# Kernel optimization log

Measured on AMD Instinct MI355X. Metric: run time of the kernel, lower is better.

## Reference

```python
import jax, jax.numpy as jnp
import numpy as np
from jax import lax

B, S, T = 32, 128, 128
V_SRC, V_TGT, E, U = 32000, 32000, 128, 256


def _lstm(xs, h0, c0, Wx, Wh, b):
    # xs: [T, B, F]; Keras gate order i, f, g(candidate), o
    def step(carry, x):
        h, c = carry
        z = x @ Wx + h @ Wh + b
        i, f, g, o = jnp.split(z, 4, axis=-1)
        c = jax.nn.sigmoid(f) * c + jax.nn.sigmoid(i) * jnp.tanh(g)
        h = jax.nn.sigmoid(o) * jnp.tanh(c)
        return (h, c), h
    (h, c), hs = lax.scan(step, (h0, c0), xs)
    return hs, h, c


def setup_inputs() -> dict:
    key = jax.random.key(0)
    ks = jax.random.split(key, 20)
    p = lambda k, shp: (jax.random.normal(k, shp, dtype=jnp.float32) * 0.02)
    return {
        "src": jax.random.randint(ks[0], (B, S), 0, V_SRC),
        "tgt": jax.random.randint(ks[1], (B, T), 0, V_TGT),
        "enc_emb": p(ks[2], (V_SRC, E)),
        "enc_Wx": p(ks[3], (E, 4 * U)),
        "enc_Wh": p(ks[4], (U, 4 * U)),
        "enc_b": jnp.zeros((4 * U,), jnp.float32),
        "dec_emb": p(ks[5], (V_TGT, E)),
        "dec_Wx": p(ks[6], (U + E, 4 * U)),
        "dec_Wh": p(ks[7], (U, 4 * U)),
        "dec_b": jnp.zeros((4 * U,), jnp.float32),
        "att_W1": p(ks[8], (U, U)),
        "att_b1": jnp.zeros((U,), jnp.float32),
        "att_W2": p(ks[9], (U, U)),
        "att_b2": jnp.zeros((U,), jnp.float32),
        "att_V": p(ks[10], (U, 1)),
        "att_bV": jnp.zeros((1,), jnp.float32),
        "fc_W": p(ks[11], (U, V_TGT)),
        "fc_b": jnp.zeros((V_TGT,), jnp.float32),
    }


def reference(src, tgt, enc_emb, enc_Wx, enc_Wh, enc_b, dec_emb, dec_Wx, dec_Wh,
              dec_b, att_W1, att_b1, att_W2, att_b2, att_V, att_bV, fc_W, fc_b):
    # ---- encoder ----
    enc_x = enc_emb[src]                                  # [B,S,E]
    enc_hs, h, c = _lstm(enc_x.transpose(1, 0, 2),
                         jnp.zeros((B, U), enc_Wx.dtype),
                         jnp.zeros((B, U), enc_Wx.dtype),
                         enc_Wx, enc_Wh, enc_b)
    enc_out = enc_hs.transpose(1, 0, 2)                   # [B,S,U]
    keys = enc_out @ att_W2 + att_b2                      # [B,S,U] (hoisted, same math)

    # ---- decoder (faithful: step 0 uses tgt[:,0]; step t>=1 uses tgt[:,t-1]) ----
    dec_tokens = jnp.concatenate([tgt[:, :1], tgt[:, :-1]], axis=1)  # [B,T]
    dec_x = dec_emb[dec_tokens].transpose(1, 0, 2)        # [T,B,E]

    def step(carry, x_emb):
        h, c = carry
        q = (h @ att_W1 + att_b1)[:, None, :]             # [B,1,U]
        score = jnp.tanh(q + keys) @ att_V + att_bV       # [B,S,1]
        attn = jax.nn.softmax(score, axis=1)
        ctx = jnp.sum(attn * enc_out, axis=1)             # [B,U]
        xin = jnp.concatenate([ctx, x_emb], axis=-1)      # [B,U+E]
        z = xin @ dec_Wx + h @ dec_Wh + dec_b
        i, f, g, o = jnp.split(z, 4, axis=-1)
        c = jax.nn.sigmoid(f) * c + jax.nn.sigmoid(i) * jnp.tanh(g)
        h = jax.nn.sigmoid(o) * jnp.tanh(c)
        probs = jax.nn.softmax(h @ fc_W + fc_b, axis=-1)  # [B,V]
        return (h, c), probs

    _, out = lax.scan(step, (h, c), dec_x)                # [T,B,V]
    return out.transpose(1, 0, 2)                         # [B,T,V]
```

## Files before the change

kernel.cpp:

```cpp
#include <hip/hip_runtime.h>
#include <hip/hip_bf16.h>
#include <hip/hip_fp16.h>
#include <cstdint>
#include <cstddef>

#define B_ 32
#define S_ 128
#define T_ 128
#define E_ 128
#define U_ 256
#define V_ 32000
#define G4 1024
#define TV 4096000

typedef __attribute__((ext_vector_type(8))) short short8_t;
typedef __attribute__((ext_vector_type(4))) float f32x4;
typedef unsigned long long u64;

static __device__ __forceinline__ unsigned short f2bf(float x) {
  union { float f; unsigned int u; } v; v.f = x;
  unsigned int r = (v.u + 0x7fffu + ((v.u >> 16) & 1u)) >> 16;
  return (unsigned short)r;
}
static __device__ __forceinline__ float sigmoidf_(float x) {
  return 1.0f / (1.0f + __expf(-x));
}
static __device__ __forceinline__ float tanhf_(float x) {
  float e = __expf(2.0f * x);
  return 1.0f - 2.0f / (e + 1.0f);
}

static __device__ __forceinline__ unsigned int f2e5(float x) {
  __half h = __float2half(x);
  __half_raw hr = *(__half_raw*)&h;
  unsigned int u = hr.x;
  unsigned int r = (u + 0x7Fu + ((u >> 8) & 1u)) >> 8;
  return r & 0xFFu;
}

static __device__ __forceinline__ unsigned pk2(float a, float b) {
  auto h = __builtin_amdgcn_cvt_pkrtz(a, b);
  return __builtin_bit_cast(unsigned, h);
}
#define SEL01 0x05000400u
#define SEL23 0x07000600u
static __device__ __forceinline__ unsigned e5pair(unsigned w, unsigned sel) {
  return __builtin_amdgcn_perm(w, 0u, sel);
}
static __device__ __forceinline__ float dot2(unsigned a, unsigned b, float c) {
  float d;
  asm("v_dot2_f32_f16 %0, %1, %2, %3" : "=v"(d) : "v"(a), "v"(b), "v"(c));
  return d;
}
static __device__ __forceinline__ unsigned pkadd(unsigned a, unsigned b) {
  unsigned d; asm("v_pk_add_f16 %0, %1, %2" : "=v"(d) : "v"(a), "v"(b)); return d;
}
static __device__ __forceinline__ unsigned pkmul(unsigned a, unsigned b) {
  unsigned d; asm("v_pk_mul_f16 %0, %1, %2" : "=v"(d) : "v"(a), "v"(b)); return d;
}
static __device__ __forceinline__ unsigned pkfma(unsigned a, unsigned b, unsigned c) {
  unsigned d; asm("v_pk_fma_f16 %0, %1, %2, %3" : "=v"(d) : "v"(a), "v"(b), "v"(c)); return d;
}
static __device__ __forceinline__ unsigned pkmax(unsigned a, unsigned b) {
  unsigned d; asm("v_pk_max_f16 %0, %1, %2" : "=v"(d) : "v"(a), "v"(b)); return d;
}
static __device__ __forceinline__ unsigned pkmin(unsigned a, unsigned b) {
  unsigned d; asm("v_pk_min_f16 %0, %1, %2" : "=v"(d) : "v"(a), "v"(b)); return d;
}

static __device__ __forceinline__ void pub64u(u64* p, unsigned val, unsigned tag) {
  u64 v = ((u64)tag << 32) | (u64)val;
  __hip_atomic_store(p, v, __ATOMIC_RELAXED, __HIP_MEMORY_SCOPE_AGENT);
}
static __device__ __forceinline__ u64 ld64(const u64* p) {
  return __hip_atomic_load(p, __ATOMIC_RELAXED, __HIP_MEMORY_SCOPE_AGENT);
}

__global__ __launch_bounds__(256) void k_prep_x(
    const int* __restrict__ src, const int* __restrict__ tgt,
    const float* __restrict__ enc_emb, const float* __restrict__ enc_Wx,
    const float* __restrict__ enc_b,
    const float* __restrict__ dec_emb, const float* __restrict__ dec_Wx,
    const float* __restrict__ dec_b,
    float* __restrict__ Xe, float* __restrict__ Xd)
{
  __shared__ float emb_l[8][E_];
  int wg = blockIdx.x;
  int tid = threadIdx.x;
  bool is_dec = (wg >= 512);
  int r0 = (is_dec ? (wg - 512) : wg) * 8;
  const float* emb  = is_dec ? dec_emb : enc_emb;
  const float* W    = is_dec ? (dec_Wx + (size_t)U_ * G4) : enc_Wx;
  const float* bias = is_dec ? dec_b : enc_b;
  float* Xout = is_dec ? Xd : Xe;

  for (int i = 0; i < 4; ++i) {
    int lin = i * 256 + tid;
    int rr = lin >> 7, k = lin & 127;
    int r = r0 + rr;
    int b = r & 31, st = r >> 5;
    int tok;
    if (is_dec) tok = tgt[b * T_ + (st > 0 ? st - 1 : 0)];
    else        tok = src[b * S_ + st];
    emb_l[rr][k] = emb[(size_t)tok * E_ + k];
  }
  __syncthreads();

  float acc[8][4];
  #pragma unroll
  for (int rr = 0; rr < 8; ++rr)
    #pragma unroll
    for (int cc = 0; cc < 4; ++cc) acc[rr][cc] = 0.f;

  for (int k = 0; k < E_; ++k) {
    float w0 = W[(size_t)k * G4 + tid];
    float w1 = W[(size_t)k * G4 + tid + 256];
    float w2 = W[(size_t)k * G4 + tid + 512];
    float w3 = W[(size_t)k * G4 + tid + 768];
    #pragma unroll
    for (int rr = 0; rr < 8; ++rr) {
      float e = emb_l[rr][k];
      acc[rr][0] += e * w0; acc[rr][1] += e * w1;
      acc[rr][2] += e * w2; acc[rr][3] += e * w3;
    }
  }
  #pragma unroll
  for (int rr = 0; rr < 8; ++rr) {
    int r = r0 + rr;
    #pragma unroll
    for (int cc = 0; cc < 4; ++cc) {
      int col = tid + cc * 256;
      Xout[(size_t)r * G4 + col] = acc[rr][cc] + bias[col];
    }
  }
}

__global__ __launch_bounds__(256) void k_prep_fcw(
    const float* __restrict__ fcW, unsigned short* __restrict__ fcWt)
{
  __shared__ float tile[64][65];
  int bid = blockIdx.x, tid = threadIdx.x;
  int n0 = (bid % 500) * 64, k0 = (bid / 500) * 64;
  for (int i = 0; i < 16; ++i) {
    int lin = i * 256 + tid;
    int k = lin >> 6, n = lin & 63;
    tile[k][n] = fcW[(size_t)(k0 + k) * V_ + n0 + n];
  }
  __syncthreads();
  for (int i = 0; i < 16; ++i) {
    int lin = i * 256 + tid;
    int n = lin >> 6, k = lin & 63;
    fcWt[(size_t)(n0 + n) * 256 + k0 + k] = f2bf(tile[k][n]);
  }
}

__global__ __launch_bounds__(1024) void k_encoder8(
    const float* __restrict__ Xe, const float* __restrict__ Wh,
    float* __restrict__ enc_out, float* __restrict__ h_state,
    float* __restrict__ c_state, u64* __restrict__ hpubE )
{
  __shared__ unsigned int WhU[64 * 128];
  __shared__ unsigned int h2[128];
  __shared__ float scr_z[8 * 128];

  int bid = blockIdx.x, tid = threadIdx.x;
  int b = bid & 31, g = bid >> 5;

  for (int idx = tid; idx < 64 * 128; idx += 1024) {
    int k4 = idx >> 7, c = idx & 127;
    int gc = (c >> 5) * 256 + g * 32 + (c & 31);
    unsigned w = 0;
    #pragma unroll
    for (int i = 0; i < 4; ++i)
      w |= f2e5(Wh[(size_t)(4 * k4 + i) * G4 + gc]) << (8 * i);
    WhU[k4 * 128 + c] = w;
  }
  float c_reg = 0.f, h_reg = 0.f;
  __syncthreads();

  for (int s = 0; s < S_; ++s) {
    float xe0 = 0.f, xe1 = 0.f, xe2 = 0.f, xe3 = 0.f;
    if (tid < 32) {
      const float* xe = Xe + (size_t)(s * B_ + b) * G4 + g * 32 + tid;
      xe0 = xe[0]; xe1 = xe[256]; xe2 = xe[512]; xe3 = xe[768];
    }
    if (tid < 128) {
      if (s == 0) h2[tid] = 0u;
      else {
        const u64* p = &hpubE[((size_t)(s & 1) * 32 + b) * 128 + tid];
        u64 v = ld64(p);
        while ((unsigned)(v >> 32) < (unsigned)s) { __builtin_amdgcn_s_sleep(1); v = ld64(p); }
        h2[tid] = (unsigned)v;
      }
    }
    __syncthreads();
    {
      int c = tid & 127, k8 = tid >> 7;
      const unsigned* wp = &WhU[(k8 * 8) * 128 + c];
      const unsigned* hh = &h2[k8 * 16];
      float z0 = 0.f, z1 = 0.f;
      #pragma unroll
      for (int j = 0; j < 8; ++j) {
        unsigned w = wp[j * 128];
        z0 = dot2(e5pair(w, SEL01), hh[2 * j], z0);
        z1 = dot2(e5pair(w, SEL23), hh[2 * j + 1], z1);
      }
      scr_z[k8 * 128 + c] = z0 + z1;
    }
    __syncthreads();
    if (tid < 32) {
      int r = tid, gc = g * 32 + r;
      float z[4] = {xe0, xe1, xe2, xe3};
      #pragma unroll
      for (int q = 0; q < 4; ++q) {
        int c = q * 32 + r;
        #pragma unroll
        for (int k8 = 0; k8 < 8; ++k8) z[q] += scr_z[k8 * 128 + c];
      }
      float c = sigmoidf_(z[1]) * c_reg + sigmoidf_(z[0]) * tanhf_(z[2]);
      c_reg = c;
      float h = sigmoidf_(z[3]) * tanhf_(c);
      h_reg = h;
      enc_out[((size_t)(b * S_ + s)) * U_ + gc] = h;
      if (s < S_ - 1) {
        float hx = __shfl_xor(h, 1);
        if (!(r & 1))
          pub64u(&hpubE[((size_t)((s + 1) & 1) * 32 + b) * 128 + g * 16 + (r >> 1)],
                 pk2(h, hx), (unsigned)(s + 1));
      }
    }
    __syncthreads();
  }
  if (tid < 32) {
    h_state[b * U_ + g * 32 + tid] = h_reg;
    c_state[b * U_ + g * 32 + tid] = c_reg;
  }
}

__global__ __launch_bounds__(256) void k_keys(
    const float* __restrict__ enc_out, const float* __restrict__ W2,
    const float* __restrict__ b2,
    unsigned char* __restrict__ keys8, unsigned char* __restrict__ eo8T)
{
  __shared__ float x_l[8][U_];
  int wg = blockIdx.x, tid = threadIdx.x;
  int r0 = wg * 8;
  for (int i = 0; i < 8; ++i) x_l[i][tid] = enc_out[(size_t)(r0 + i) * U_ + tid];
  __syncthreads();
  float acc[8];
  #pragma unroll
  for (int rr = 0; rr < 8; ++rr) acc[rr] = 0.f;
  for (int k = 0; k < U_; ++k) {
    float w = W2[(size_t)k * U_ + tid];
    #pragma unroll
    for (int rr = 0; rr < 8; ++rr) acc[rr] += x_l[rr][k] * w;
  }
  float bb = b2[tid];
  #pragma unroll
  for (int rr = 0; rr < 8; ++rr) {
    int r = r0 + rr;
    keys8[(size_t)r * U_ + tid] = (unsigned char)f2e5(acc[rr] + bb);
    int bI = r >> 7, sI = r & 127;
    eo8T[((size_t)bI * U_ + tid) * S_ + sI] = (unsigned char)f2e5(x_l[rr][tid]);
  }
}

__global__ __launch_bounds__(1024) void k_decoder(
    const float* __restrict__ Xd, const float* __restrict__ dec_Wx,
    const float* __restrict__ Wh,
    const float* __restrict__ W1, const float* __restrict__ b1,
    const float* __restrict__ attV, const float* __restrict__ attbV,
    const unsigned char* __restrict__ keys8, const unsigned char* __restrict__ eo8T,
    const float* __restrict__ h0, const float* __restrict__ c0,
    unsigned short* __restrict__ Hbf,
    u64* __restrict__ hpub2 )
{
  __shared__ unsigned int WxU[64 * 128];
  __shared__ unsigned int WhU[64 * 128];
  __shared__ unsigned int W1U[64 * 256];
  __shared__ float scr_q[4 * 256];
  __shared__ float scr_c[4 * 256];
  __shared__ float scr_z[8 * 128];
  __shared__ unsigned int q2[160];
  __shared__ unsigned int aV2[160];
  __shared__ unsigned int h2[128];
  __shared__ unsigned int ctx2[128];
  __shared__ unsigned int esc2[64];
  __shared__ float escw[16];
  __shared__ float b1_l[256];

  int bid = blockIdx.x, tid = threadIdx.x;
  int b = bid & 31, g = bid >> 5;
  int lane = tid & 63, wid = tid >> 6;

  for (int idx = tid; idx < 64 * 128; idx += 1024) {
    int k4 = idx >> 7, c = idx & 127;
    int gc = (c >> 5) * 256 + g * 32 + (c & 31);
    unsigned wx = 0, wh = 0;
    #pragma unroll
    for (int i = 0; i < 4; ++i) {
      int k = 4 * k4 + i;
      wx |= f2e5(dec_Wx[(size_t)k * G4 + gc]) << (8 * i);
      wh |= f2e5(Wh[(size_t)k * G4 + gc]) << (8 * i);
    }
    WxU[k4 * 128 + c] = wx;
    WhU[k4 * 128 + c] = wh;
  }
  for (int idx = tid; idx < 64 * 256; idx += 1024) {
    int k4 = idx >> 8, u = idx & 255;
    unsigned w = 0;
    #pragma unroll
    for (int i = 0; i < 4; ++i)
      w |= f2e5(W1[(size_t)(4 * k4 + i) * U_ + u]) << (8 * i);
    W1U[k4 * 256 + u] = w;
  }
  if (tid < 128) {
    int p = tid;
    aV2[(p >> 4) * 20 + (p & 15)] = pk2(attV[2 * p], attV[2 * p + 1]);
  }
  if (tid < 256) b1_l[tid] = b1[tid];
  float bV = attbV[0];
  float c_reg = 0.f, h_reg = 0.f;
  if (tid < 32) {
    h_reg = h0[b * U_ + g * 32 + tid];
    c_reg = c0[b * U_ + g * 32 + tid];
  }
  __syncthreads();

  if (tid < 32) {
    float hx = __shfl_xor(h_reg, 1);
    if (!(tid & 1))
      pub64u(&hpub2[((size_t)0 * 32 + b) * 128 + g * 16 + (tid >> 1)], pk2(h_reg, hx), 1u);
  }

  const unsigned NEG1 = pk2(-1.f, -1.f), POS1 = pk2(1.f, 1.f);
  const unsigned C1 = pk2(-0.333333333f, -0.333333333f);
  const unsigned C2 = pk2(0.133333333f, 0.133333333f);
  const unsigned C3 = pk2(-0.053968254f, -0.053968254f);

  const unsigned char* kb = keys8 + (size_t)b * S_ * U_;
  const unsigned char* eb = eo8T + (size_t)b * U_ * S_;

  for (int t = 0; t < T_; ++t) {
    unsigned tag = (unsigned)(t + 1);
    int par = t & 1;

    float xd0 = 0.f, xd1 = 0.f, xd2 = 0.f, xd3 = 0.f;
    if (tid < 32) {
      const float* xd = Xd + (size_t)(t * B_ + b) * G4 + g * 32 + tid;
      xd0 = xd[0]; xd1 = xd[256]; xd2 = xd[512]; xd3 = xd[768];
    }

    if (tid < 128) {
      const u64* hp = &hpub2[((size_t)par * 32 + b) * 128 + tid];
      u64 vh = ld64(hp);
      while ((unsigned)(vh >> 32) < tag) { __builtin_amdgcn_s_sleep(1); vh = ld64(hp); }
      h2[tid] = (unsigned)vh;
    }
    __syncthreads();

    int sI = tid >> 3, uo = tid & 7;
    int uI = tid & 255, sq = tid >> 8;
    uint4 kA, kB, eA, eB;
    {
      const uint4* kp = (const uint4*)(kb + (size_t)sI * U_ + uo * 32);
      kA = kp[0]; kB = kp[1];
      const uint4* ep = (const uint4*)(eb + (size_t)uI * S_ + sq * 32);
      eA = ep[0]; eB = ep[1];
    }
    {
      int c = tid & 255, kq = tid >> 8;
      const unsigned* wp = &W1U[(kq * 16) * 256 + c];
      const unsigned* hh = &h2[kq * 32];
      float qa = 0.f, qb = 0.f;
      #pragma unroll
      for (int j = 0; j < 16; ++j) {
        unsigned w = wp[j * 256];
        qa = dot2(e5pair(w, SEL01), hh[2 * j], qa);
        qb = dot2(e5pair(w, SEL23), hh[2 * j + 1], qb);
      }
      scr_q[kq * 256 + c] = qa + qb;
    }
    __syncthreads();

    if (tid < 128) {
      int u0 = 2 * tid;
      float q0 = scr_q[u0] + scr_q[256 + u0] + scr_q[512 + u0] + scr_q[768 + u0] + b1_l[u0];
      float q1 = scr_q[u0 + 1] + scr_q[256 + u0 + 1] + scr_q[512 + u0 + 1] + scr_q[768 + u0 + 1] + b1_l[u0 + 1];
      q2[(tid >> 4) * 20 + (tid & 15)] = pk2(q0, q1);
    }
    __syncthreads();

    {
      unsigned kw[8] = {kA.x, kA.y, kA.z, kA.w, kB.x, kB.y, kB.z, kB.w};
      const unsigned* qq = &q2[uo * 20];
      const unsigned* vv = &aV2[uo * 20];
      float a0 = 0.f, a1 = 0.f;
      #pragma unroll
      for (int j = 0; j < 8; ++j) {
        unsigned w = kw[j];
        unsigned x0 = pkadd(e5pair(w, SEL01), qq[2 * j]);
        unsigned x1 = pkadd(e5pair(w, SEL23), qq[2 * j + 1]);
        x0 = pkmin(pkmax(x0, NEG1), POS1);
        x1 = pkmin(pkmax(x1, NEG1), POS1);
        unsigned s0_ = pkmul(x0, x0), s1_ = pkmul(x1, x1);
        unsigned t0 = pkfma(s0_, C3, C2), t1 = pkfma(s1_, C3, C2);
        t0 = pkfma(s0_, t0, C1); t1 = pkfma(s1_, t1, C1);
        unsigned th0 = pkfma(pkmul(x0, s0_), t0, x0);
        unsigned th1 = pkfma(pkmul(x1, s1_), t1, x1);
        a0 = dot2(th0, vv[2 * j], a0);
        a1 = dot2(th1, vv[2 * j + 1], a1);
      }
      float a = a0 + a1;
      a += __shfl_xor(a, 1); a += __shfl_xor(a, 2); a += __shfl_xor(a, 4);
      float ea = __expf(a + bV);
      float ep = __shfl_xor(ea, 8);
      if (uo == 0 && !(sI & 1)) esc2[sI >> 1] = pk2(ea, ep);
      float dsum = ea;
      dsum += __shfl_xor(dsum, 8); dsum += __shfl_xor(dsum, 16); dsum += __shfl_xor(dsum, 32);
      if (lane == 0) escw[wid] = dsum;
    }
    __syncthreads();

    {
      unsigned ewv[8] = {eA.x, eA.y, eA.z, eA.w, eB.x, eB.y, eB.z, eB.w};
      const unsigned* e2 = &esc2[sq * 16];
      float c0a = 0.f, c1a = 0.f;
      #pragma unroll
      for (int j = 0; j < 8; ++j) {
        unsigned w = ewv[j];
        c0a = dot2(e5pair(w, SEL01), e2[2 * j], c0a);
        c1a = dot2(e5pair(w, SEL23), e2[2 * j + 1], c1a);
      }
      scr_c[sq * 256 + uI] = c0a + c1a;
    }
    __syncthreads();

    if (tid < 128) {
      int u0 = 2 * tid;
      float ca = scr_c[u0] + scr_c[256 + u0] + scr_c[512 + u0] + scr_c[768 + u0];
      float cb = scr_c[u0 + 1] + scr_c[256 + u0 + 1] + scr_c[512 + u0 + 1] + scr_c[768 + u0 + 1];
      ctx2[tid] = pk2(ca, cb);
    }
    __syncthreads();

    {
      float d = ((escw[0] + escw[1]) + (escw[2] + escw[3])) +
                ((escw[4] + escw[5]) + (escw[6] + escw[7])) +
                ((escw[8] + escw[9]) + (escw[10] + escw[11])) +
                ((escw[12] + escw[13]) + (escw[14] + escw[15]));
      float dinv = 1.0f / d;
      int c = tid & 127, k8 = tid >> 7;
      const unsigned* wxp = &WxU[(k8 * 8) * 128 + c];
      const unsigned* whp = &WhU[(k8 * 8) * 128 + c];
      const unsigned* cc = &ctx2[k8 * 16];
      const unsigned* hh = &h2[k8 * 16];
      float zx0 = 0.f, zx1 = 0.f, zh0 = 0.f, zh1 = 0.f;
      #pragma unroll
      for (int j = 0; j < 8; ++j) {
        unsigned wx = wxp[j * 128], wh = whp[j * 128];
        zx0 = dot2(e5pair(wx, SEL01), cc[2 * j], zx0);
        zx1 = dot2(e5pair(wx, SEL23), cc[2 * j + 1], zx1);
        zh0 = dot2(e5pair(wh, SEL01), hh[2 * j], zh0);
        zh1 = dot2(e5pair(wh, SEL23), hh[2 * j + 1], zh1);
      }
      scr_z[k8 * 128 + c] = (zh0 + zh1) + (zx0 + zx1) * dinv;
    }
    __syncthreads();

    if (tid < 32) {
      int r = tid, gc = g * 32 + r;
      float z[4] = {xd0, xd1, xd2, xd3};
      #pragma unroll
      for (int q = 0; q < 4; ++q) {
        int c = q * 32 + r;
        #pragma unroll
        for (int k8 = 0; k8 < 8; ++k8) z[q] += scr_z[k8 * 128 + c];
      }
      float c = sigmoidf_(z[1]) * c_reg + sigmoidf_(z[0]) * tanhf_(z[2]);
      c_reg = c;
      float h = sigmoidf_(z[3]) * tanhf_(c);
      h_reg = h;
      Hbf[(size_t)(t * B_ + b) * U_ + gc] = f2bf(h);
      if (t < T_ - 1) {
        int par1 = (t + 1) & 1;
        float hx = __shfl_xor(h, 1);
        if (!(r & 1))
          pub64u(&hpub2[((size_t)par1 * 32 + b) * 128 + g * 16 + (r >> 1)],
                 pk2(h, hx), (unsigned)(t + 2));
      }
    }
    __syncthreads();
  }
}

__global__ __launch_bounds__(256) void k_fc(
    const unsigned short* __restrict__ Hbf, const unsigned short* __restrict__ fcWt,
    const float* __restrict__ fcb, float* __restrict__ out,
    float* __restrict__ rs_part)
{
  __shared__ uint4 Al[128 * 8];
  __shared__ uint4 Bl[128 * 8];
  __shared__ float rsum_l[128][2];

  int bid = blockIdx.x, tid = threadIdx.x;
  int nt = bid >> 5, mt = bid & 31;
  int m0 = mt * 128, n0 = nt * 128;
  int lane = tid & 63, wave = tid >> 6;
  int wm = (wave >> 1) * 64, wn = (wave & 1) * 64;
  int g = lane >> 4, r15 = lane & 15;

  f32x4 acc[4][4];
  f32x4 zero = {0.f, 0.f, 0.f, 0.f};
  #pragma unroll
  for (int mi = 0; mi < 4; ++mi)
    #pragma unroll
    for (int ni = 0; ni < 4; ++ni) acc[mi][ni] = zero;

  const unsigned short* Ag = Hbf  + (size_t)m0 * 256;
  const unsigned short* Bg = fcWt + (size_t)n0 * 256;

  for (int kt = 0; kt < 4; ++kt) {
    int kk = kt * 64;
    #pragma unroll
    for (int blk = 0; blk < 4; ++blk) {
      int lin = blk * 256 + tid;
      int row = lin >> 3, kq = lin & 7;
      Al[row * 8 + (kq ^ (row & 7))] = *(const uint4*)(Ag + (size_t)row * 256 + kk + kq * 8);
      Bl[row * 8 + (kq ^ (row & 7))] = *(const uint4*)(Bg + (size_t)row * 256 + kk + kq * 8);
    }
    __syncthreads();
    #pragma unroll
    for (int kk2 = 0; kk2 < 2; ++kk2) {
      short8_t a[4], bfr[4];
      #pragma unroll
      for (int mi = 0; mi < 4; ++mi) {
        int row = wm + mi * 16 + r15;
        a[mi] = *(const short8_t*)&Al[row * 8 + ((kk2 * 4 + g) ^ (row & 7))];
      }
      #pragma unroll
      for (int ni = 0; ni < 4; ++ni) {
        int row = wn + ni * 16 + r15;
        bfr[ni] = *(const short8_t*)&Bl[row * 8 + ((kk2 * 4 + g) ^ (row & 7))];
      }
      #pragma unroll
      for (int mi = 0; mi < 4; ++mi)
        #pragma unroll
        for (int ni = 0; ni < 4; ++ni)
          acc[mi][ni] = __builtin_amdgcn_mfma_f32_16x16x32_bf16(a[mi], bfr[ni], acc[mi][ni], 0, 0, 0);
    }
    __syncthreads();
  }

  float fcb_l[4];
  #pragma unroll
  for (int ni = 0; ni < 4; ++ni) fcb_l[ni] = fcb[n0 + wn + ni * 16 + r15];

  #pragma unroll
  for (int mi = 0; mi < 4; ++mi) {
    #pragma unroll
    for (int jj = 0; jj < 4; ++jj) {
      int rloc = wm + mi * 16 + g * 4 + jj;
      int grow = m0 + rloc;
      int bb = grow & 31, tt = grow >> 5;
      size_t obase = (size_t)bb * TV + (size_t)tt * V_;
      float s = 0.f;
      #pragma unroll
      for (int ni = 0; ni < 4; ++ni) {
        float v = __expf(acc[mi][ni][jj] + fcb_l[ni]);
        out[obase + n0 + wn + ni * 16 + r15] = v;
        s += v;
      }
      s += __shfl_xor(s, 1); s += __shfl_xor(s, 2);
      s += __shfl_xor(s, 4); s += __shfl_xor(s, 8);
      if (r15 == 0) rsum_l[rloc][wave & 1] = s;
    }
  }
  __syncthreads();
  if (tid < 128)
    rs_part[(size_t)nt * 4096 + m0 + tid] = rsum_l[tid][0] + rsum_l[tid][1];
}

__global__ __launch_bounds__(256) void k_rowsum(
    const float* __restrict__ rs_part, float* __restrict__ row_inv)
{
  int gidx = blockIdx.x * 256 + threadIdx.x;
  float s = 0.f;
  for (int nt = 0; nt < 250; ++nt) s += rs_part[(size_t)nt * 4096 + gidx];
  row_inv[gidx] = 1.0f / s;
}

__global__ __launch_bounds__(256) void k_norm(
    float4* __restrict__ out4, const float* __restrict__ row_inv)
{
  const long total = 32768000;
  long stride = (long)gridDim.x * 256;
  for (long i = (long)blockIdx.x * 256 + threadIdx.x; i < total; i += stride) {
    long flat = i * 4;
    int bb = (int)(flat / TV);
    int rem = (int)(flat % TV);
    int tt = rem / V_;
    float sc = row_inv[tt * 32 + bb];
    float4 v = out4[i];
    v.x *= sc; v.y *= sc; v.z *= sc; v.w *= sc;
    out4[i] = v;
  }
}

extern "C" void kernel_launch(void* const* d_in, const int* in_sizes, int n_in,
                              void* d_out, int out_size, void* d_ws, size_t ws_size,
                              hipStream_t stream) {
  (void)in_sizes; (void)n_in; (void)out_size; (void)ws_size;
  const int*   src     = (const int*)d_in[0];
  const int*   tgt     = (const int*)d_in[1];
  const float* enc_emb = (const float*)d_in[2];
  const float* enc_Wx  = (const float*)d_in[3];
  const float* enc_Wh  = (const float*)d_in[4];
  const float* enc_b   = (const float*)d_in[5];
  const float* dec_emb = (const float*)d_in[6];
  const float* dec_Wx  = (const float*)d_in[7];
  const float* dec_Wh  = (const float*)d_in[8];
  const float* dec_b   = (const float*)d_in[9];
  const float* att_W1  = (const float*)d_in[10];
  const float* att_b1  = (const float*)d_in[11];
  const float* att_W2  = (const float*)d_in[12];
  const float* att_b2  = (const float*)d_in[13];
  const float* att_V   = (const float*)d_in[14];
  const float* att_bV  = (const float*)d_in[15];
  const float* fc_W    = (const float*)d_in[16];
  const float* fc_b    = (const float*)d_in[17];
  float* out = (float*)d_out;

  char* ws = (char*)d_ws;
  size_t o = 0;
  auto alloc = [&](size_t bytes) {
    char* p = ws + o;
    o = (o + bytes + 255) & ~(size_t)255;
    return p;
  };
  float*          Xe      = (float*)alloc((size_t)S_ * B_ * G4 * 4);
  float*          Xd      = (float*)alloc((size_t)T_ * B_ * G4 * 4);
  float*          enc_out = (float*)alloc((size_t)B_ * S_ * U_ * 4);
  unsigned char*  keys8   = (unsigned char*)alloc((size_t)B_ * S_ * U_);
  unsigned char*  eo8T    = (unsigned char*)alloc((size_t)B_ * U_ * S_);
  unsigned short* Hbf     = (unsigned short*)alloc((size_t)T_ * B_ * U_ * 2);
  unsigned short* fcWt    = (unsigned short*)alloc((size_t)V_ * U_ * 2);
  float*          h_state = (float*)alloc((size_t)B_ * U_ * 4);
  float*          c_state = (float*)alloc((size_t)B_ * U_ * 4);
  float*          rs_part = (float*)alloc((size_t)250 * 4096 * 4);
  float*          row_inv = (float*)alloc((size_t)4096 * 4);
  size_t pub_off = o;
  u64* hpubE = (u64*)alloc((size_t)2 * 32 * 128 * 8);
  u64* hpub2 = (u64*)alloc((size_t)2 * 32 * 128 * 8);
  size_t pub_bytes = o - pub_off;

  hipMemsetAsync(ws + pub_off, 0, pub_bytes, stream);
  hipLaunchKernelGGL(k_prep_x, dim3(1024), dim3(256), 0, stream,
                     src, tgt, enc_emb, enc_Wx, enc_b, dec_emb, dec_Wx, dec_b, Xe, Xd);
  hipLaunchKernelGGL(k_prep_fcw, dim3(2000), dim3(256), 0, stream, fc_W, fcWt);
  hipLaunchKernelGGL(k_encoder8, dim3(256), dim3(1024), 0, stream,
                     Xe, enc_Wh, enc_out, h_state, c_state, hpubE);
  hipLaunchKernelGGL(k_keys, dim3(512), dim3(256), 0, stream,
                     enc_out, att_W2, att_b2, keys8, eo8T);
  hipLaunchKernelGGL(k_decoder, dim3(256), dim3(1024), 0, stream,
                     Xd, dec_Wx, dec_Wh, att_W1, att_b1, att_V, att_bV,
                     keys8, eo8T, h_state, c_state, Hbf, hpub2);
  hipLaunchKernelGGL(k_fc, dim3(8000), dim3(256), 0, stream,
                     Hbf, fcWt, fc_b, out, rs_part);
  hipLaunchKernelGGL(k_rowsum, dim3(16), dim3(256), 0, stream, rs_part, row_inv);
  hipLaunchKernelGGL(k_norm, dim3(2048), dim3(256), 0, stream,
                     (float4*)d_out, row_inv);
}
```

Before: 1.430 ms.

## Replace LDS partial-sum reductions with wave shuffles and fold h-wait into step tail

The encoder and decoder recurrent steps now split each dot product so the partial sums for one output column sit in adjacent lanes. They reduce those partials with xor-shuffles instead of writing them to shared scratch and summing in a separate phase, which removes a barrier per reduction. The shared weight tiles get a padded row stride (129/257) to avoid bank conflicts under the new access pattern. The spin-wait for the next hidden state now runs at the end of each step, so it shares the existing trailing barrier and one barrier per step goes away.

```diff
diff --git a/kernel.cpp b/kernel.cpp
--- a/kernel.cpp
+++ b/kernel.cpp
@@ -154,14 +154,14 @@
   }
 }
 
-__global__ __launch_bounds__(1024) void k_encoder8(
+__global__ __launch_bounds__(1024) void k_encoder(
     const float* __restrict__ Xe, const float* __restrict__ Wh,
     float* __restrict__ enc_out, float* __restrict__ h_state,
     float* __restrict__ c_state, u64* __restrict__ hpubE )
 {
-  __shared__ unsigned int WhU[64 * 128];
+  __shared__ unsigned int WhU[64 * 129];
   __shared__ unsigned int h2[128];
-  __shared__ float scr_z[8 * 128];
+  __shared__ float zfull[128];
 
   int bid = blockIdx.x, tid = threadIdx.x;
   int b = bid & 31, g = bid >> 5;
@@ -173,8 +173,9 @@
     #pragma unroll
     for (int i = 0; i < 4; ++i)
       w |= f2e5(Wh[(size_t)(4 * k4 + i) * G4 + gc]) << (8 * i);
-    WhU[k4 * 128 + c] = w;
-  }
+    WhU[k4 * 129 + c] = w;
+  }
+  if (tid < 128) h2[tid] = 0u;
   float c_reg = 0.f, h_reg = 0.f;
   __syncthreads();
 
@@ -184,42 +185,31 @@
       const float* xe = Xe + (size_t)(s * B_ + b) * G4 + g * 32 + tid;
       xe0 = xe[0]; xe1 = xe[256]; xe2 = xe[512]; xe3 = xe[768];
     }
-    if (tid < 128) {
-      if (s == 0) h2[tid] = 0u;
-      else {
-        const u64* p = &hpubE[((size_t)(s & 1) * 32 + b) * 128 + tid];
-        u64 v = ld64(p);
-        while ((unsigned)(v >> 32) < (unsigned)s) { __builtin_amdgcn_s_sleep(1); v = ld64(p); }
-        h2[tid] = (unsigned)v;
-      }
-    }
-    __syncthreads();
     {
-      int c = tid & 127, k8 = tid >> 7;
-      const unsigned* wp = &WhU[(k8 * 8) * 128 + c];
+      int c = tid >> 3, k8 = tid & 7;
+      const unsigned* wp = &WhU[(k8 * 8) * 129 + c];
       const unsigned* hh = &h2[k8 * 16];
       float z0 = 0.f, z1 = 0.f;
       #pragma unroll
       for (int j = 0; j < 8; ++j) {
-        unsigned w = wp[j * 128];
+        unsigned w = wp[j * 129];
         z0 = dot2(e5pair(w, SEL01), hh[2 * j], z0);
         z1 = dot2(e5pair(w, SEL23), hh[2 * j + 1], z1);
       }
-      scr_z[k8 * 128 + c] = z0 + z1;
+      float z = z0 + z1;
+      z += __shfl_xor(z, 1); z += __shfl_xor(z, 2); z += __shfl_xor(z, 4);
+      if ((tid & 7) == 0) zfull[c] = z;
     }
     __syncthreads();
     if (tid < 32) {
       int r = tid, gc = g * 32 + r;
-      float z[4] = {xe0, xe1, xe2, xe3};
-      #pragma unroll
-      for (int q = 0; q < 4; ++q) {
-        int c = q * 32 + r;
-        #pragma unroll
-        for (int k8 = 0; k8 < 8; ++k8) z[q] += scr_z[k8 * 128 + c];
-      }
-      float c = sigmoidf_(z[1]) * c_reg + sigmoidf_(z[0]) * tanhf_(z[2]);
+      float zi = zfull[r] + xe0;
+      float zf = zfull[32 + r] + xe1;
+      float zg = zfull[64 + r] + xe2;
+      float zo = zfull[96 + r] + xe3;
+      float c = sigmoidf_(zf) * c_reg + sigmoidf_(zi) * tanhf_(zg);
       c_reg = c;
-      float h = sigmoidf_(z[3]) * tanhf_(c);
+      float h = sigmoidf_(zo) * tanhf_(c);
       h_reg = h;
       enc_out[((size_t)(b * S_ + s)) * U_ + gc] = h;
       if (s < S_ - 1) {
@@ -228,6 +218,12 @@
           pub64u(&hpubE[((size_t)((s + 1) & 1) * 32 + b) * 128 + g * 16 + (r >> 1)],
                  pk2(h, hx), (unsigned)(s + 1));
       }
+    }
+    if (s < S_ - 1 && tid < 128) {
+      const u64* p = &hpubE[((size_t)((s + 1) & 1) * 32 + b) * 128 + tid];
+      u64 v = ld64(p);
+      while ((unsigned)(v >> 32) < (unsigned)(s + 1)) { __builtin_amdgcn_s_sleep(1); v = ld64(p); }
+      h2[tid] = (unsigned)v;
     }
     __syncthreads();
   }
@@ -275,18 +271,16 @@
     unsigned short* __restrict__ Hbf,
     u64* __restrict__ hpub2 )
 {
-  __shared__ unsigned int WxU[64 * 128];
-  __shared__ unsigned int WhU[64 * 128];
-  __shared__ unsigned int W1U[64 * 256];
-  __shared__ float scr_q[4 * 256];
-  __shared__ float scr_c[4 * 256];
-  __shared__ float scr_z[8 * 128];
+  __shared__ unsigned int WxU[64 * 129];
+  __shared__ unsigned int WhU[64 * 129];
+  __shared__ unsigned int W1U[64 * 257];
   __shared__ unsigned int q2[160];
   __shared__ unsigned int aV2[160];
   __shared__ unsigned int h2[128];
   __shared__ unsigned int ctx2[128];
   __shared__ unsigned int esc2[64];
   __shared__ float escw[16];
+  __shared__ float zfull[128];
   __shared__ float b1_l[256];
 
   int bid = blockIdx.x, tid = threadIdx.x;
@@ -303,8 +297,8 @@
       wx |= f2e5(dec_Wx[(size_t)k * G4 + gc]) << (8 * i);
       wh |= f2e5(Wh[(size_t)k * G4 + gc]) << (8 * i);
     }
-    WxU[k4 * 128 + c] = wx;
-    WhU[k4 * 128 + c] = wh;
+    WxU[k4 * 129 + c] = wx;
+    WhU[k4 * 129 + c] = wh;
   }
   for (int idx = tid; idx < 64 * 256; idx += 1024) {
     int k4 = idx >> 8, u = idx & 255;
@@ -312,12 +306,10 @@
     #pragma unroll
     for (int i = 0; i < 4; ++i)
       w |= f2e5(W1[(size_t)(4 * k4 + i) * U_ + u]) << (8 * i);
-    W1U[k4 * 256 + u] = w;
-  }
-  if (tid < 128) {
-    int p = tid;
-    aV2[(p >> 4) * 20 + (p & 15)] = pk2(attV[2 * p], attV[2 * p + 1]);
-  }
+    W1U[k4 * 257 + u] = w;
+  }
+  if (tid < 128)
+    aV2[(tid >> 4) * 20 + (tid & 15)] = pk2(attV[2 * tid], attV[2 * tid + 1]);
   if (tid < 256) b1_l[tid] = b1[tid];
   float bV = attbV[0];
   float c_reg = 0.f, h_reg = 0.f;
@@ -332,6 +324,13 @@
     if (!(tid & 1))
       pub64u(&hpub2[((size_t)0 * 32 + b) * 128 + g * 16 + (tid >> 1)], pk2(h_reg, hx), 1u);
   }
+  if (tid < 128) {
+    const u64* hp = &hpub2[((size_t)0 * 32 + b) * 128 + tid];
+    u64 vh = ld64(hp);
+    while ((unsigned)(vh >> 32) < 1u) { __builtin_amdgcn_s_sleep(1); vh = ld64(hp); }
+    h2[tid] = (unsigned)vh;
+  }
+  __syncthreads();
 
   const unsigned NEG1 = pk2(-1.f, -1.f), POS1 = pk2(1.f, 1.f);
   const unsigned C1 = pk2(-0.333333333f, -0.333333333f);
@@ -342,25 +341,14 @@
   const unsigned char* eb = eo8T + (size_t)b * U_ * S_;
 
   for (int t = 0; t < T_; ++t) {
-    unsigned tag = (unsigned)(t + 1);
-    int par = t & 1;
-
     float xd0 = 0.f, xd1 = 0.f, xd2 = 0.f, xd3 = 0.f;
     if (tid < 32) {
       const float* xd = Xd + (size_t)(t * B_ + b) * G4 + g * 32 + tid;
       xd0 = xd[0]; xd1 = xd[256]; xd2 = xd[512]; xd3 = xd[768];
     }
 
-    if (tid < 128) {
-      const u64* hp = &hpub2[((size_t)par * 32 + b) * 128 + tid];
-      u64 vh = ld64(hp);
-      while ((unsigned)(vh >> 32) < tag) { __builtin_amdgcn_s_sleep(1); vh = ld64(hp); }
-      h2[tid] = (unsigned)vh;
-    }
-    __syncthreads();
-
     int sI = tid >> 3, uo = tid & 7;
-    int uI = tid & 255, sq = tid >> 8;
+    int uI = tid >> 2, sq = tid & 3;
     uint4 kA, kB, eA, eB;
     {
       const uint4* kp = (const uint4*)(kb + (size_t)sI * U_ + uo * 32);
@@ -369,25 +357,24 @@
       eA = ep[0]; eB = ep[1];
     }
     {
-      int c = tid & 255, kq = tid >> 8;
-      const unsigned* wp = &W1U[(kq * 16) * 256 + c];
+      int u = uI, kq = sq;
+      const unsigned* wp = &W1U[(kq * 16) * 257 + u];
       const unsigned* hh = &h2[kq * 32];
       float qa = 0.f, qb = 0.f;
       #pragma unroll
       for (int j = 0; j < 16; ++j) {
-        unsigned w = wp[j * 256];
+        unsigned w = wp[j * 257];
         qa = dot2(e5pair(w, SEL01), hh[2 * j], qa);
         qb = dot2(e5pair(w, SEL23), hh[2 * j + 1], qb);
       }
-      scr_q[kq * 256 + c] = qa + qb;
-    }
-    __syncthreads();
-
-    if (tid < 128) {
-      int u0 = 2 * tid;
-      float q0 = scr_q[u0] + scr_q[256 + u0] + scr_q[512 + u0] + scr_q[768 + u0] + b1_l[u0];
-      float q1 = scr_q[u0 + 1] + scr_q[256 + u0 + 1] + scr_q[512 + u0 + 1] + scr_q[768 + u0 + 1] + b1_l[u0 + 1];
-      q2[(tid >> 4) * 20 + (tid & 15)] = pk2(q0, q1);
+      float q = qa + qb;
+      q += __shfl_xor(q, 1); q += __shfl_xor(q, 2);
+      q += b1_l[u];
+      float qx = __shfl_xor(q, 4);
+      if ((tid & 7) == 0) {
+        int p = u >> 1;
+        q2[(p >> 4) * 20 + (p & 15)] = pk2(q, qx);
+      }
     }
     __syncthreads();
 
@@ -432,15 +419,10 @@
         c0a = dot2(e5pair(w, SEL01), e2[2 * j], c0a);
         c1a = dot2(e5pair(w, SEL23), e2[2 * j + 1], c1a);
       }
-      scr_c[sq * 256 + uI] = c0a + c1a;
-    }
-    __syncthreads();
-
-    if (tid < 128) {
-      int u0 = 2 * tid;
-      float ca = scr_c[u0] + scr_c[256 + u0] + scr_c[512 + u0] + scr_c[768 + u0];
-      float cb = scr_c[u0 + 1] + scr_c[256 + u0 + 1] + scr_c[512 + u0 + 1] + scr_c[768 + u0 + 1];
-      ctx2[tid] = pk2(ca, cb);
+      float ca = c0a + c1a;
+      ca += __shfl_xor(ca, 1); ca += __shfl_xor(ca, 2);
+      float cx = __shfl_xor(ca, 4);
+      if ((tid & 7) == 0) ctx2[uI >> 1] = pk2(ca, cx);
     }
     __syncthreads();
 
@@ -450,36 +432,35 @@
                 ((escw[8] + escw[9]) + (escw[10] + escw[11])) +
                 ((escw[12] + escw[13]) + (escw[14] + escw[15]));
       float dinv = 1.0f / d;
-      int c = tid & 127, k8 = tid >> 7;
-      const unsigned* wxp = &WxU[(k8 * 8) * 128 + c];
-      const unsigned* whp = &WhU[(k8 * 8) * 128 + c];
+      int c = tid >> 3, k8 = tid & 7;
+      const unsigned* wxp = &WxU[(k8 * 8) * 129 + c];
+      const unsigned* whp = &WhU[(k8 * 8) * 129 + c];
       const unsigned* cc = &ctx2[k8 * 16];
       const unsigned* hh = &h2[k8 * 16];
       float zx0 = 0.f, zx1 = 0.f, zh0 = 0.f, zh1 = 0.f;
       #pragma unroll
       for (int j = 0; j < 8; ++j) {
-        unsigned wx = wxp[j * 128], wh = whp[j * 128];
+        unsigned wx = wxp[j * 129], wh = whp[j * 129];
         zx0 = dot2(e5pair(wx, SEL01), cc[2 * j], zx0);
         zx1 = dot2(e5pair(wx, SEL23), cc[2 * j + 1], zx1);
         zh0 = dot2(e5pair(wh, SEL01), hh[2 * j], zh0);
         zh1 = dot2(e5pair(wh, SEL23), hh[2 * j + 1], zh1);
       }
-      scr_z[k8 * 128 + c] = (zh0 + zh1) + (zx0 + zx1) * dinv;
+      float z = (zh0 + zh1) + (zx0 + zx1) * dinv;
+      z += __shfl_xor(z, 1); z += __shfl_xor(z, 2); z += __shfl_xor(z, 4);
+      if ((tid & 7) == 0) zfull[c] = z;
     }
     __syncthreads();
 
     if (tid < 32) {
       int r = tid, gc = g * 32 + r;
-      float z[4] = {xd0, xd1, xd2, xd3};
-      #pragma unroll
-      for (int q = 0; q < 4; ++q) {
-        int c = q * 32 + r;
-        #pragma unroll
-        for (int k8 = 0; k8 < 8; ++k8) z[q] += scr_z[k8 * 128 + c];
-      }
-      float c = sigmoidf_(z[1]) * c_reg + sigmoidf_(z[0]) * tanhf_(z[2]);
+      float zi = zfull[r] + xd0;
+      float zf = zfull[32 + r] + xd1;
+      float zg = zfull[64 + r] + xd2;
+      float zo = zfull[96 + r] + xd3;
+      float c = sigmoidf_(zf) * c_reg + sigmoidf_(zi) * tanhf_(zg);
       c_reg = c;
-      float h = sigmoidf_(z[3]) * tanhf_(c);
+      float h = sigmoidf_(zo) * tanhf_(c);
       h_reg = h;
       Hbf[(size_t)(t * B_ + b) * U_ + gc] = f2bf(h);
       if (t < T_ - 1) {
@@ -489,6 +470,14 @@
           pub64u(&hpub2[((size_t)par1 * 32 + b) * 128 + g * 16 + (r >> 1)],
                  pk2(h, hx), (unsigned)(t + 2));
       }
+    }
+    if (t < T_ - 1 && tid < 128) {
+      int par1 = (t + 1) & 1;
+      unsigned tag2 = (unsigned)(t + 2);
+      const u64* hp = &hpub2[((size_t)par1 * 32 + b) * 128 + tid];
+      u64 vh = ld64(hp);
+      while ((unsigned)(vh >> 32) < tag2) { __builtin_amdgcn_s_sleep(1); vh = ld64(hp); }
+      h2[tid] = (unsigned)vh;
     }
     __syncthreads();
   }
@@ -658,7 +647,7 @@
   hipLaunchKernelGGL(k_prep_x, dim3(1024), dim3(256), 0, stream,
                      src, tgt, enc_emb, enc_Wx, enc_b, dec_emb, dec_Wx, dec_b, Xe, Xd);
   hipLaunchKernelGGL(k_prep_fcw, dim3(2000), dim3(256), 0, stream, fc_W, fcWt);
-  hipLaunchKernelGGL(k_encoder8, dim3(256), dim3(1024), 0, stream,
+  hipLaunchKernelGGL(k_encoder, dim3(256), dim3(1024), 0, stream,
                      Xe, enc_Wh, enc_out, h_state, c_state, hpubE);
   hipLaunchKernelGGL(k_keys, dim3(512), dim3(256), 0, stream,
                      enc_out, att_W2, att_b2, keys8, eo8T);
```

Result: slower. 1.902 ms (+33.0%).

## Stage unnormalized softmax exps in bf16 and move h-wait to end of step

Applied to the files above, without the earlier changes.

The FC kernel now writes the exponentials as bf16 into a workspace buffer, when one fits, instead of fp32 into the output. A new normalize kernel reads the bf16 values and writes the scaled fp32 output. This halves the intermediate write and read traffic of the 500MB output pass, at the cost of bf16 rounding in the probabilities. Separately, the encoder and decoder loops poll for the next hidden state at the end of each step, which removes one __syncthreads per step. Whether the bf16 path runs depends on the workspace size.

```diff
diff --git a/kernel.cpp b/kernel.cpp
--- a/kernel.cpp
+++ b/kernel.cpp
@@ -14,6 +14,7 @@
 #define TV 4096000
 
 typedef __attribute__((ext_vector_type(8))) short short8_t;
+typedef __attribute__((ext_vector_type(8))) unsigned short ushort8_t;
 typedef __attribute__((ext_vector_type(4))) float f32x4;
 typedef unsigned long long u64;
 
@@ -21,6 +22,9 @@
   union { float f; unsigned int u; } v; v.f = x;
   unsigned int r = (v.u + 0x7fffu + ((v.u >> 16) & 1u)) >> 16;
   return (unsigned short)r;
+}
+static __device__ __forceinline__ float bf2f(unsigned short u) {
+  return __uint_as_float(((unsigned)u) << 16);
 }
 static __device__ __forceinline__ float sigmoidf_(float x) {
   return 1.0f / (1.0f + __expf(-x));
@@ -175,6 +179,7 @@
       w |= f2e5(Wh[(size_t)(4 * k4 + i) * G4 + gc]) << (8 * i);
     WhU[k4 * 128 + c] = w;
   }
+  if (tid < 128) h2[tid] = 0u;
   float c_reg = 0.f, h_reg = 0.f;
   __syncthreads();
 
@@ -184,16 +189,6 @@
       const float* xe = Xe + (size_t)(s * B_ + b) * G4 + g * 32 + tid;
       xe0 = xe[0]; xe1 = xe[256]; xe2 = xe[512]; xe3 = xe[768];
     }
-    if (tid < 128) {
-      if (s == 0) h2[tid] = 0u;
-      else {
-        const u64* p = &hpubE[((size_t)(s & 1) * 32 + b) * 128 + tid];
-        u64 v = ld64(p);
-        while ((unsigned)(v >> 32) < (unsigned)s) { __builtin_amdgcn_s_sleep(1); v = ld64(p); }
-        h2[tid] = (unsigned)v;
-      }
-    }
-    __syncthreads();
     {
       int c = tid & 127, k8 = tid >> 7;
       const unsigned* wp = &WhU[(k8 * 8) * 128 + c];
@@ -228,6 +223,12 @@
           pub64u(&hpubE[((size_t)((s + 1) & 1) * 32 + b) * 128 + g * 16 + (r >> 1)],
                  pk2(h, hx), (unsigned)(s + 1));
       }
+    }
+    if (s < S_ - 1 && tid < 128) {
+      const u64* p = &hpubE[((size_t)((s + 1) & 1) * 32 + b) * 128 + tid];
+      u64 v = ld64(p);
+      while ((unsigned)(v >> 32) < (unsigned)(s + 1)) { __builtin_amdgcn_s_sleep(1); v = ld64(p); }
+      h2[tid] = (unsigned)v;
     }
     __syncthreads();
   }
@@ -332,6 +333,13 @@
     if (!(tid & 1))
       pub64u(&hpub2[((size_t)0 * 32 + b) * 128 + g * 16 + (tid >> 1)], pk2(h_reg, hx), 1u);
   }
+  if (tid < 128) {
+    const u64* hp = &hpub2[((size_t)0 * 32 + b) * 128 + tid];
+    u64 vh = ld64(hp);
+    while ((unsigned)(vh >> 32) < 1u) { __builtin_amdgcn_s_sleep(1); vh = ld64(hp); }
+    h2[tid] = (unsigned)vh;
+  }
+  __syncthreads();
 
   const unsigned NEG1 = pk2(-1.f, -1.f), POS1 = pk2(1.f, 1.f);
   const unsigned C1 = pk2(-0.333333333f, -0.333333333f);
@@ -342,22 +350,11 @@
   const unsigned char* eb = eo8T + (size_t)b * U_ * S_;
 
   for (int t = 0; t < T_; ++t) {
-    unsigned tag = (unsigned)(t + 1);
-    int par = t & 1;
-
     float xd0 = 0.f, xd1 = 0.f, xd2 = 0.f, xd3 = 0.f;
     if (tid < 32) {
       const float* xd = Xd + (size_t)(t * B_ + b) * G4 + g * 32 + tid;
       xd0 = xd[0]; xd1 = xd[256]; xd2 = xd[512]; xd3 = xd[768];
     }
-
-    if (tid < 128) {
-      const u64* hp = &hpub2[((size_t)par * 32 + b) * 128 + tid];
-      u64 vh = ld64(hp);
-      while ((unsigned)(vh >> 32) < tag) { __builtin_amdgcn_s_sleep(1); vh = ld64(hp); }
-      h2[tid] = (unsigned)vh;
-    }
-    __syncthreads();
 
     int sI = tid >> 3, uo = tid & 7;
     int uI = tid & 255, sq = tid >> 8;
@@ -490,6 +487,14 @@
                  pk2(h, hx), (unsigned)(t + 2));
       }
     }
+    if (t < T_ - 1 && tid < 128) {
+      int par1 = (t + 1) & 1;
+      unsigned tag2 = (unsigned)(t + 2);
+      const u64* hp = &hpub2[((size_t)par1 * 32 + b) * 128 + tid];
+      u64 vh = ld64(hp);
+      while ((unsigned)(vh >> 32) < tag2) { __builtin_amdgcn_s_sleep(1); vh = ld64(hp); }
+      h2[tid] = (unsigned)vh;
+    }
     __syncthreads();
   }
 }
@@ -497,6 +502,7 @@
 __global__ __launch_bounds__(256) void k_fc(
     const unsigned short* __restrict__ Hbf, const unsigned short* __restrict__ fcWt,
     const float* __restrict__ fcb, float* __restrict__ out,
+    unsigned short* __restrict__ expv,
     float* __restrict__ rs_part)
 {
   __shared__ uint4 Al[128 * 8];
@@ -565,11 +571,21 @@
       int bb = grow & 31, tt = grow >> 5;
       size_t obase = (size_t)bb * TV + (size_t)tt * V_;
       float s = 0.f;
-      #pragma unroll
-      for (int ni = 0; ni < 4; ++ni) {
-        float v = __expf(acc[mi][ni][jj] + fcb_l[ni]);
-        out[obase + n0 + wn + ni * 16 + r15] = v;
-        s += v;
+      if (expv) {
+        #pragma unroll
+        for (int ni = 0; ni < 4; ++ni) {
+          float v = __expf(acc[mi][ni][jj] + fcb_l[ni]);
+          unsigned short us = f2bf(v);
+          expv[obase + n0 + wn + ni * 16 + r15] = us;
+          s += bf2f(us);
+        }
+      } else {
+        #pragma unroll
+        for (int ni = 0; ni < 4; ++ni) {
+          float v = __expf(acc[mi][ni][jj] + fcb_l[ni]);
+          out[obase + n0 + wn + ni * 16 + r15] = v;
+          s += v;
+        }
       }
       s += __shfl_xor(s, 1); s += __shfl_xor(s, 2);
       s += __shfl_xor(s, 4); s += __shfl_xor(s, 8);
@@ -588,6 +604,29 @@
   float s = 0.f;
   for (int nt = 0; nt < 250; ++nt) s += rs_part[(size_t)nt * 4096 + gidx];
   row_inv[gidx] = 1.0f / s;
+}
+
+__global__ __launch_bounds__(256) void k_norm_bf16(
+    const unsigned short* __restrict__ expv, float* __restrict__ out,
+    const float* __restrict__ row_inv)
+{
+  const long total = 16384000;
+  long stride = (long)gridDim.x * 256;
+  for (long i = (long)blockIdx.x * 256 + threadIdx.x; i < total; i += stride) {
+    long flat = i * 8;
+    int bb = (int)(flat / TV);
+    int rem = (int)(flat % TV);
+    int tt = rem / V_;
+    float sc = row_inv[tt * 32 + bb];
+    ushort8_t v = *(const ushort8_t*)&expv[flat];
+    float4 o0, o1;
+    o0.x = bf2f(v[0]) * sc; o0.y = bf2f(v[1]) * sc;
+    o0.z = bf2f(v[2]) * sc; o0.w = bf2f(v[3]) * sc;
+    o1.x = bf2f(v[4]) * sc; o1.y = bf2f(v[5]) * sc;
+    o1.z = bf2f(v[6]) * sc; o1.w = bf2f(v[7]) * sc;
+    *(float4*)&out[flat] = o0;
+    *(float4*)&out[flat + 4] = o1;
+  }
 }
 
 __global__ __launch_bounds__(256) void k_norm(
@@ -610,7 +649,7 @@
 extern "C" void kernel_launch(void* const* d_in, const int* in_sizes, int n_in,
                               void* d_out, int out_size, void* d_ws, size_t ws_size,
                               hipStream_t stream) {
-  (void)in_sizes; (void)n_in; (void)out_size; (void)ws_size;
+  (void)in_sizes; (void)n_in; (void)out_size;
   const int*   src     = (const int*)d_in[0];
   const int*   tgt     = (const int*)d_in[1];
   const float* enc_emb = (const float*)d_in[2];
@@ -653,6 +692,10 @@
   u64* hpubE = (u64*)alloc((size_t)2 * 32 * 128 * 8);
   u64* hpub2 = (u64*)alloc((size_t)2 * 32 * 128 * 8);
   size_t pub_bytes = o - pub_off;
+  size_t expv_bytes = (size_t)B_ * T_ * V_ * 2;
+  unsigned short* expv = nullptr;
+  if (o + expv_bytes <= ws_size)
+    expv = (unsigned short*)alloc(expv_bytes);
 
   hipMemsetAsync(ws + pub_off, 0, pub_bytes, stream);
   hipLaunchKernelGGL(k_prep_x, dim3(1024), dim3(256), 0, stream,
@@ -666,8 +709,12 @@
                      Xd, dec_Wx, dec_Wh, att_W1, att_b1, att_V, att_bV,
                      keys8, eo8T, h_state, c_state, Hbf, hpub2);
   hipLaunchKernelGGL(k_fc, dim3(8000), dim3(256), 0, stream,
-                     Hbf, fcWt, fc_b, out, rs_part);
+                     Hbf, fcWt, fc_b, out, expv, rs_part);
   hipLaunchKernelGGL(k_rowsum, dim3(16), dim3(256), 0, stream, rs_part, row_inv);
-  hipLaunchKernelGGL(k_norm, dim3(2048), dim3(256), 0, stream,
-                     (float4*)d_out, row_inv);
-}
+  if (expv)
+    hipLaunchKernelGGL(k_norm_bf16, dim3(4096), dim3(256), 0, stream,
+                       expv, out, row_inv);
+  else
+    hipLaunchKernelGGL(k_norm, dim3(2048), dim3(256), 0, stream,
+                       (float4*)d_out, row_inv);
+}
```

After: 1.336 ms. 1.07x faster.
